# Kernel tuning notes

Hardware: AMD Instinct MI355X
Metric: run time of the kernel (lower is better)

## Reference

```python
import jax, jax.numpy as jnp
import numpy as np

TOP_K = 2
N_TOKENS = 8192
S1_ROWS = N_TOKENS * TOP_K  # 16384
S2_ROWS = 4096
D_MODEL = 4096


def setup_inputs() -> dict:
    key = jax.random.key(0)
    k1, k2, k3, k4, k5 = jax.random.split(key, 5)
    dout_exp = jax.random.normal(k1, (S1_ROWS + S2_ROWS, D_MODEL), dtype=jnp.float32)
    weights = jax.random.uniform(k2, (S1_ROWS,), dtype=jnp.float32)
    indices_s1 = jax.random.randint(k3, (S1_ROWS,), 0, S1_ROWS, dtype=jnp.int32)
    indices_s2 = jax.random.randint(k4, (S2_ROWS,), 0, S1_ROWS, dtype=jnp.int32)
    s1exp_to_s2_indices = jax.random.randint(k5, (S2_ROWS,), 0, S1_ROWS, dtype=jnp.int32)
    return {
        "dout_exp": dout_exp,
        "weights": weights,
        "indices_s1": indices_s1,
        "indices_s2": indices_s2,
        "s1exp_to_s2_indices": s1exp_to_s2_indices,
        "n_tokens": N_TOKENS,
    }


def reference(dout_exp, weights, indices_s1, indices_s2, s1exp_to_s2_indices, n_tokens):
    # Single-rank semantics: _AllToAllSingle with matching splits is identity.
    s1_rows = indices_s1.shape[0]
    # Gather per-row combine weights for both stages.
    w_s1 = weights[indices_s1]                      # [S1]
    w_s2 = weights[indices_s2]                      # [S2]
    # Split expert output rows into stage-1 and stage-2 blocks.
    dout_s1_exp = dout_exp[:s1_rows]                # [S1, D]
    dout_s2 = dout_exp[s1_rows:]                    # [S2, D]
    # Weighted scale.
    weighted_s1 = dout_s1_exp * w_s1[:, None]       # [S1, D]
    weighted_s2 = dout_s2 * w_s2[:, None]           # [S2, D]
    # s2 -> s1 scatter-add: accumulate stage-2 rows into stage-1 row slots.
    combined_s1 = weighted_s1.at[s1exp_to_s2_indices].add(weighted_s2)  # [S1, D]
    # Final token-combine scatter: token id = flat top-k index // top_k.
    token_ids = indices_s1 // TOP_K                 # [S1]
    out = jnp.zeros((n_tokens, dout_exp.shape[1]), dtype=dout_exp.dtype)
    out = out.at[token_ids].add(combined_s1)        # [n_tokens, D]
    return out
```

## Files before the change

### kernel.cpp

```cpp
#include <hip/hip_runtime.h>

#define TOPK_SHIFT 1
#define BUCKET_CAP 24

typedef float f32x4 __attribute__((ext_vector_type(4)));

struct Entry { int src; float w; };

__global__ void bucket_kernel(
    const int* __restrict__ indices_s1,
    const int* __restrict__ indices_s2,
    const int* __restrict__ s1_to_s2,
    const float* __restrict__ weights,
    int S1, int NE,
    int* __restrict__ cursors,
    Entry* __restrict__ buckets)
{
    int i = blockIdx.x * blockDim.x + threadIdx.x;
    if (i >= NE) return;
    int token;
    float w;
    if (i < S1) {
        int idx = indices_s1[i];
        token = idx >> TOPK_SHIFT;
        w = weights[idx];
    } else {
        int j = i - S1;
        token = indices_s1[s1_to_s2[j]] >> TOPK_SHIFT;
        w = weights[indices_s2[j]];
    }
    int pos = atomicAdd(&cursors[token], 1);
    if (pos < BUCKET_CAP) {
        Entry e; e.src = i; e.w = w;
        buckets[token * BUCKET_CAP + pos] = e;
    }
}

__global__ __launch_bounds__(256) void gather_kernel(
    const f32x4* __restrict__ dout,
    const int*   __restrict__ cursors,
    const Entry* __restrict__ buckets,
    f32x4*       __restrict__ out,
    int D4)
{
    const int t   = blockIdx.x;
    const int tid = threadIdx.x;
    int n = cursors[t];
    n = (n < BUCKET_CAP) ? n : BUCKET_CAP;
    const Entry* b = buckets + t * BUCKET_CAP;

    if ((D4 & 1023) == 0) {
        for (int base = 0; base < D4; base += 1024) {
            f32x4 a0 = 0, a1 = 0, a2 = 0, a3 = 0;
            for (int e = 0; e < n; ++e) {
                const Entry en = b[e];
                const float w = en.w;
                const f32x4* row = dout + (size_t)en.src * (size_t)D4 + base;
                f32x4 v0 = __builtin_nontemporal_load(row + tid);
                f32x4 v1 = __builtin_nontemporal_load(row + tid + 256);
                f32x4 v2 = __builtin_nontemporal_load(row + tid + 512);
                f32x4 v3 = __builtin_nontemporal_load(row + tid + 768);
                a0 += w * v0;
                a1 += w * v1;
                a2 += w * v2;
                a3 += w * v3;
            }
            f32x4* orow = out + (size_t)t * (size_t)D4 + base;
            __builtin_nontemporal_store(a0, orow + tid);
            __builtin_nontemporal_store(a1, orow + tid + 256);
            __builtin_nontemporal_store(a2, orow + tid + 512);
            __builtin_nontemporal_store(a3, orow + tid + 768);
        }
    } else {
        for (int c = tid; c < D4; c += 256) {
            f32x4 acc = 0;
            for (int e = 0; e < n; ++e)
                acc += b[e].w * __builtin_nontemporal_load(
                           dout + (size_t)b[e].src * (size_t)D4 + c);
            __builtin_nontemporal_store(acc, out + (size_t)t * (size_t)D4 + c);
        }
    }
}

extern "C" void kernel_launch(void* const* d_in, const int* in_sizes, int n_in,
                              void* d_out, int out_size, void* d_ws, size_t ws_size,
                              hipStream_t stream) {
    const float* dout_exp   = (const float*)d_in[0];
    const float* weights    = (const float*)d_in[1];
    const int*   indices_s1 = (const int*)d_in[2];
    const int*   indices_s2 = (const int*)d_in[3];
    const int*   s1_to_s2   = (const int*)d_in[4];

    const int S1    = in_sizes[1];
    const int S2    = in_sizes[3];
    const int NROWS = S1 + S2;
    const int D     = in_sizes[0] / NROWS;
    const int NT    = out_size / D;
    const int D4    = D / 4;
    const int NE    = NROWS;

    int*   cursors = (int*)d_ws;
    Entry* buckets = (Entry*)(cursors + NT);

    (void)hipMemsetAsync(cursors, 0, (size_t)NT * sizeof(int), stream);

    const int threads = 256;
    const int eblocks = (NE + threads - 1) / threads;

    bucket_kernel<<<eblocks, threads, 0, stream>>>(
        indices_s1, indices_s2, s1_to_s2, weights, S1, NE,
        cursors, buckets);

    gather_kernel<<<NT, 256, 0, stream>>>(
        (const f32x4*)dout_exp, cursors, buckets,
        (f32x4*)d_out, D4);
}
```

Baseline: 99.88 us.

## Fuse memset, bucketing and gather into one cooperative persistent kernel

Replaces the memset plus two kernel launches with a single cooperative kernel of 1024 persistent blocks that zeroes the cursors, builds the per-token buckets, and then gathers. Grid-wide syncs separate the phases. The aim is to remove launch gaps and inter-kernel idle time. In exchange, the gather now runs on a fixed persistent grid with about 8 tokens per block, and the grid syncs add overhead. The cooperative launch also fails if 1024 blocks cannot be co-resident.

New measurement: 268.7 us. +169.0%, slower.

```diff
diff --git a/kernel.cpp b/kernel.cpp
--- a/kernel.cpp
+++ b/kernel.cpp
@@ -1,83 +1,94 @@
 #include <hip/hip_runtime.h>
+#include <hip/hip_cooperative_groups.h>
+
+namespace cg = cooperative_groups;
 
 #define TOPK_SHIFT 1
 #define BUCKET_CAP 24
+#define GRID_BLKS 1024
 
 typedef float f32x4 __attribute__((ext_vector_type(4)));
 
 struct Entry { int src; float w; };
 
-__global__ void bucket_kernel(
+__global__ __launch_bounds__(256) void fused_kernel(
     const int* __restrict__ indices_s1,
     const int* __restrict__ indices_s2,
     const int* __restrict__ s1_to_s2,
     const float* __restrict__ weights,
-    int S1, int NE,
+    const f32x4* __restrict__ dout,
+    f32x4* __restrict__ out,
     int* __restrict__ cursors,
-    Entry* __restrict__ buckets)
+    Entry* __restrict__ buckets,
+    int S1, int NE, int NT, int D4)
 {
-    int i = blockIdx.x * blockDim.x + threadIdx.x;
-    if (i >= NE) return;
-    int token;
-    float w;
-    if (i < S1) {
-        int idx = indices_s1[i];
-        token = idx >> TOPK_SHIFT;
-        w = weights[idx];
-    } else {
-        int j = i - S1;
-        token = indices_s1[s1_to_s2[j]] >> TOPK_SHIFT;
-        w = weights[indices_s2[j]];
+    cg::grid_group grid = cg::this_grid();
+    const int gtid    = blockIdx.x * blockDim.x + threadIdx.x;
+    const int gthreads = gridDim.x * blockDim.x;
+
+    for (int i = gtid; i < NT; i += gthreads) cursors[i] = 0;
+    grid.sync();
+
+    for (int i = gtid; i < NE; i += gthreads) {
+        int token;
+        float w;
+        if (i < S1) {
+            int idx = indices_s1[i];
+            token = idx >> TOPK_SHIFT;
+            w = weights[idx];
+        } else {
+            int j = i - S1;
+            token = indices_s1[s1_to_s2[j]] >> TOPK_SHIFT;
+            w = weights[indices_s2[j]];
+        }
+        int pos = atomicAdd(&cursors[token], 1);
+        if (pos < BUCKET_CAP) {
+            Entry e; e.src = i; e.w = w;
+            buckets[token * BUCKET_CAP + pos] = e;
+        }
     }
-    int pos = atomicAdd(&cursors[token], 1);
-    if (pos < BUCKET_CAP) {
-        Entry e; e.src = i; e.w = w;
-        buckets[token * BUCKET_CAP + pos] = e;
-    }
-}
+    grid.sync();
 
-__global__ __launch_bounds__(256) void gather_kernel(
-    const f32x4* __restrict__ dout,
-    const int*   __restrict__ cursors,
-    const Entry* __restrict__ buckets,
-    f32x4*       __restrict__ out,
-    int D4)
-{
-    const int t   = blockIdx.x;
     const int tid = threadIdx.x;
-    int n = cursors[t];
-    n = (n < BUCKET_CAP) ? n : BUCKET_CAP;
-    const Entry* b = buckets + t * BUCKET_CAP;
-
     if ((D4 & 1023) == 0) {
-        for (int base = 0; base < D4; base += 1024) {
-            f32x4 a0 = 0, a1 = 0, a2 = 0, a3 = 0;
-            for (int e = 0; e < n; ++e) {
-                const Entry en = b[e];
-                const float w = en.w;
-                const f32x4* row = dout + (size_t)en.src * (size_t)D4 + base;
-                f32x4 v0 = __builtin_nontemporal_load(row + tid);
-                f32x4 v1 = __builtin_nontemporal_load(row + tid + 256);
-                f32x4 v2 = __builtin_nontemporal_load(row + tid + 512);
-                f32x4 v3 = __builtin_nontemporal_load(row + tid + 768);
-                a0 += w * v0;
-                a1 += w * v1;
-                a2 += w * v2;
-                a3 += w * v3;
+        for (int t = blockIdx.x; t < NT; t += gridDim.x) {
+            int n = cursors[t];
+            n = (n < BUCKET_CAP) ? n : BUCKET_CAP;
+            const Entry* b = buckets + t * BUCKET_CAP;
+            for (int base = 0; base < D4; base += 1024) {
+                f32x4 a0 = 0, a1 = 0, a2 = 0, a3 = 0;
+                for (int e = 0; e < n; ++e) {
+                    const Entry en = b[e];
+                    const float w = en.w;
+                    const f32x4* row = dout + (size_t)en.src * (size_t)D4 + base;
+                    f32x4 v0 = __builtin_nontemporal_load(row + tid);
+                    f32x4 v1 = __builtin_nontemporal_load(row + tid + 256);
+                    f32x4 v2 = __builtin_nontemporal_load(row + tid + 512);
+                    f32x4 v3 = __builtin_nontemporal_load(row + tid + 768);
+                    a0 += w * v0;
+                    a1 += w * v1;
+                    a2 += w * v2;
+                    a3 += w * v3;
+                }
+                f32x4* orow = out + (size_t)t * (size_t)D4 + base;
+                __builtin_nontemporal_store(a0, orow + tid);
+                __builtin_nontemporal_store(a1, orow + tid + 256);
+                __builtin_nontemporal_store(a2, orow + tid + 512);
+                __builtin_nontemporal_store(a3, orow + tid + 768);
             }
-            f32x4* orow = out + (size_t)t * (size_t)D4 + base;
-            __builtin_nontemporal_store(a0, orow + tid);
-            __builtin_nontemporal_store(a1, orow + tid + 256);
-            __builtin_nontemporal_store(a2, orow + tid + 512);
-            __builtin_nontemporal_store(a3, orow + tid + 768);
         }
     } else {
-        for (int c = tid; c < D4; c += 256) {
-            f32x4 acc = 0;
-            for (int e = 0; e < n; ++e)
-                acc += b[e].w * __builtin_nontemporal_load(
-                           dout + (size_t)b[e].src * (size_t)D4 + c);
-            __builtin_nontemporal_store(acc, out + (size_t)t * (size_t)D4 + c);
+        for (int t = blockIdx.x; t < NT; t += gridDim.x) {
+            int n = cursors[t];
+            n = (n < BUCKET_CAP) ? n : BUCKET_CAP;
+            const Entry* b = buckets + t * BUCKET_CAP;
+            for (int c = tid; c < D4; c += 256) {
+                f32x4 acc = 0;
+                for (int e = 0; e < n; ++e)
+                    acc += b[e].w * __builtin_nontemporal_load(
+                               dout + (size_t)b[e].src * (size_t)D4 + c);
+                __builtin_nontemporal_store(acc, out + (size_t)t * (size_t)D4 + c);
+            }
         }
     }
 }
@@ -102,16 +113,16 @@
     int*   cursors = (int*)d_ws;
     Entry* buckets = (Entry*)(cursors + NT);
 
-    (void)hipMemsetAsync(cursors, 0, (size_t)NT * sizeof(int), stream);
+    const f32x4* dout4 = (const f32x4*)dout_exp;
+    f32x4*       out4  = (f32x4*)d_out;
 
-    const int threads = 256;
-    const int eblocks = (NE + threads - 1) / threads;
-
-    bucket_kernel<<<eblocks, threads, 0, stream>>>(
-        indices_s1, indices_s2, s1_to_s2, weights, S1, NE,
-        cursors, buckets);
-
-    gather_kernel<<<NT, 256, 0, stream>>>(
-        (const f32x4*)dout_exp, cursors, buckets,
-        (f32x4*)d_out, D4);
+    void* args[] = {
+        (void*)&indices_s1, (void*)&indices_s2, (void*)&s1_to_s2,
+        (void*)&weights, (void*)&dout4, (void*)&out4,
+        (void*)&cursors, (void*)&buckets,
+        (void*)&S1, (void*)&NE, (void*)&NT, (void*)&D4
+    };
+    (void)hipLaunchCooperativeKernel((void*)fused_kernel,
+                                     dim3(GRID_BLKS), dim3(256),
+                                     args, 0, stream);
 }
```
